# Performance work log

Hardware: AMD Instinct MI355X
Metric: run time of the kernel (lower is better)

Reference implementation:

```python
import jax, jax.numpy as jnp
import numpy as np

N0_SRC, N0_DST, E0 = 495616, 45056, 450560
N1_DST, E1 = 4096, 40960
IN_FEATS, N_HIDDEN, N_CLASSES = 256, 128, 16


def setup_inputs() -> dict:
    key = jax.random.key(0)
    ks = jax.random.split(key, 12)
    x = jax.random.normal(ks[0], (N0_SRC, IN_FEATS), dtype=jnp.float32)
    src0 = jax.random.randint(ks[1], (E0,), 0, N0_SRC, dtype=jnp.int32)
    dst0 = jax.random.randint(ks[2], (E0,), 0, N0_DST, dtype=jnp.int32)
    w0 = jax.random.uniform(ks[3], (E0,), dtype=jnp.float32)
    src1 = jax.random.randint(ks[4], (E1,), 0, N0_DST, dtype=jnp.int32)
    dst1 = jax.random.randint(ks[5], (E1,), 0, N1_DST, dtype=jnp.int32)
    w1 = jax.random.uniform(ks[6], (E1,), dtype=jnp.float32)
    # xavier-uniform-ish init for linear weights
    def xavier(k, shape):
        fan_out, fan_in = shape
        lim = jnp.sqrt(6.0 / (fan_in + fan_out))
        return jax.random.uniform(k, shape, jnp.float32, -lim, lim)
    return {
        "x": x, "src0": src0, "dst0": dst0, "w0": w0,
        "src1": src1, "dst1": dst1, "w1": w1,
        "Wn0": xavier(ks[7], (N_HIDDEN, IN_FEATS)), "bn0": jnp.zeros((N_HIDDEN,), jnp.float32),
        "Wn1": xavier(ks[8], (N_HIDDEN, N_HIDDEN)), "bn1": jnp.zeros((N_HIDDEN,), jnp.float32),
        "Wfc": xavier(ks[9], (N_CLASSES, N_HIDDEN)), "bfc": jnp.zeros((N_CLASSES,), jnp.float32),
        "ndst0": N0_DST, "ndst1": N1_DST,
    }


def _weighted_sage_gcn(h, src, dst, w, Wn, bn, num_dst):
    """DGL-style 'gcn' SAGEConv with edge weights on a bipartite block.

    dst nodes are the prefix h[:num_dst] of the src node set.
    h_out = relu(fc_neigh((sum_e w_e*h[src_e] + h_dst) / (sum_e w_e + 1)))
    """
    h_dst = h[:num_dst]
    msg = h[src] * w[:, None]                                   # [E, D]
    agg = jax.ops.segment_sum(msg, dst, num_segments=num_dst)   # [num_dst, D]
    deg = jax.ops.segment_sum(w, dst, num_segments=num_dst)     # [num_dst]
    h_neigh = (agg + h_dst) / (deg[:, None] + 1.0)
    return jax.nn.relu(h_neigh @ Wn.T + bn)


def reference(x, src0, dst0, w0, src1, dst1, w1, Wn0, bn0, Wn1, bn1, Wfc, bfc, ndst0, ndst1):
    h = _weighted_sage_gcn(x, src0, dst0, w0, Wn0, bn0, ndst0)
    h = _weighted_sage_gcn(h, src1, dst1, w1, Wn1, bn1, ndst1)
    return h @ Wfc.T + bfc  # [ndst1, n_classes]
```

## Files before the change

kernel.cpp:

```cpp
#include <hip/hip_runtime.h>

#define N0_SRC 495616
#define N0_DST 45056
#define E0 450560
#define N1_DST 4096
#define E1 40960
#define IN_FEATS 256
#define NH 128
#define NC 16

__global__ void hist_kernel(const int* __restrict__ dst, int* __restrict__ cnt) {
    int e = blockIdx.x * blockDim.x + threadIdx.x;
    if (e < E0) atomicAdd(&cnt[dst[e]], 1);
}

__global__ void __launch_bounds__(1024) scan_kernel(int* __restrict__ cnt,
                                                    int* __restrict__ row_start) {
    __shared__ int partial[1024];
    const int CH = N0_DST / 1024;
    int t = threadIdx.x;
    int base = t * CH;
    int s = 0;
    for (int j = 0; j < CH; j++) s += cnt[base + j];
    partial[t] = s;
    __syncthreads();
    for (int off = 1; off < 1024; off <<= 1) {
        int v = (t >= off) ? partial[t - off] : 0;
        __syncthreads();
        partial[t] += v;
        __syncthreads();
    }
    int run = partial[t] - s;
    for (int j = 0; j < CH; j++) {
        int c = cnt[base + j];
        row_start[base + j] = run;
        cnt[base + j] = run;
        run += c;
    }
    if (t == 1023) row_start[N0_DST] = run;
}

__global__ void scatter_kernel(const int* __restrict__ dst, const int* __restrict__ src,
                               const float* __restrict__ w, int* __restrict__ cursor,
                               int2* __restrict__ sw) {
    int e = blockIdx.x * blockDim.x + threadIdx.x;
    if (e < E0) {
        int p = atomicAdd(&cursor[dst[e]], 1);
        sw[p] = make_int2(src[e], __float_as_int(w[e]));
    }
}

__global__ void __launch_bounds__(256) agg0_kernel(const float* __restrict__ x,
    const int2* __restrict__ sw, const int* __restrict__ row_start,
    float* __restrict__ hneigh) {
    int wv = blockIdx.x * 4 + (threadIdx.x >> 6);
    int lane = threadIdx.x & 63;
    if (wv >= N0_DST) return;
    int beg = row_start[wv], end = row_start[wv + 1];
    const float4* x4 = (const float4*)x;
    float4 xd = x4[(size_t)wv * 64 + lane];
    float ax = 0.f, ay = 0.f, az = 0.f, aw = 0.f, degs = 0.f;
    for (int i = beg; i < end; i += 4) {
        int last = end - 1;
        int i1 = (i + 1 < end) ? i + 1 : last;
        int i2 = (i + 2 < end) ? i + 2 : last;
        int i3 = (i + 3 < end) ? i + 3 : last;
        int2 p0 = sw[i];
        int2 p1 = sw[i1];
        int2 p2 = sw[i2];
        int2 p3 = sw[i3];
        float4 v0 = x4[(size_t)p0.x * 64 + lane];
        float4 v1 = x4[(size_t)p1.x * 64 + lane];
        float4 v2 = x4[(size_t)p2.x * 64 + lane];
        float4 v3 = x4[(size_t)p3.x * 64 + lane];
        float w0 = __int_as_float(p0.y);
        float w1 = (i + 1 < end) ? __int_as_float(p1.y) : 0.f;
        float w2 = (i + 2 < end) ? __int_as_float(p2.y) : 0.f;
        float w3 = (i + 3 < end) ? __int_as_float(p3.y) : 0.f;
        ax = fmaf(w0, v0.x, ax); ay = fmaf(w0, v0.y, ay);
        az = fmaf(w0, v0.z, az); aw = fmaf(w0, v0.w, aw);
        ax = fmaf(w1, v1.x, ax); ay = fmaf(w1, v1.y, ay);
        az = fmaf(w1, v1.z, az); aw = fmaf(w1, v1.w, aw);
        ax = fmaf(w2, v2.x, ax); ay = fmaf(w2, v2.y, ay);
        az = fmaf(w2, v2.z, az); aw = fmaf(w2, v2.w, aw);
        ax = fmaf(w3, v3.x, ax); ay = fmaf(w3, v3.y, ay);
        az = fmaf(w3, v3.z, az); aw = fmaf(w3, v3.w, aw);
        degs += w0 + w1 + w2 + w3;
    }
    float inv = 1.0f / (degs + 1.0f);
    float4 r;
    r.x = (ax + xd.x) * inv; r.y = (ay + xd.y) * inv;
    r.z = (az + xd.z) * inv; r.w = (aw + xd.w) * inv;
    ((float4*)hneigh)[(size_t)wv * 64 + lane] = r;
}

__global__ void __launch_bounds__(128) gemm0_kernel(const float* __restrict__ hneigh,
    const float* __restrict__ Wn, const float* __restrict__ bn,
    float* __restrict__ h0) {
    __shared__ float hn[16][IN_FEATS];
    int nb = blockIdx.x * 16;
    int tid = threadIdx.x;
    const float4* s4 = (const float4*)(hneigh + (size_t)nb * IN_FEATS);
    float4* l4 = (float4*)&hn[0][0];
    for (int i = tid; i < 16 * IN_FEATS / 4; i += 128) l4[i] = s4[i];
    __syncthreads();
    float acc[16];
#pragma unroll
    for (int n = 0; n < 16; n++) acc[n] = 0.f;
    const float4* wr4 = (const float4*)(Wn + (size_t)tid * IN_FEATS);
#pragma unroll 4
    for (int k4 = 0; k4 < IN_FEATS / 4; k4++) {
        float4 wv = wr4[k4];
        int k = k4 * 4;
#pragma unroll
        for (int n = 0; n < 16; n++) {
            acc[n] += hn[n][k + 0] * wv.x;
            acc[n] += hn[n][k + 1] * wv.y;
            acc[n] += hn[n][k + 2] * wv.z;
            acc[n] += hn[n][k + 3] * wv.w;
        }
    }
    float b = bn[tid];
#pragma unroll
    for (int n = 0; n < 16; n++) {
        float v = acc[n] + b;
        h0[(size_t)(nb + n) * NH + tid] = v > 0.f ? v : 0.f;
    }
}

__global__ void edge1_kernel(const float* __restrict__ h0,
                             const int* __restrict__ src, const int* __restrict__ dst,
                             const float* __restrict__ w,
                             float* __restrict__ agg, float* __restrict__ deg) {
    int t = blockIdx.x * blockDim.x + threadIdx.x;
    int e = t >> 5;
    int lane = t & 31;
    if (e >= E1) return;
    int s = src[e], d = dst[e];
    float we = w[e];
    float4 v = ((const float4*)(h0 + (size_t)s * NH))[lane];
    float* ad = agg + (size_t)d * NH + lane * 4;
    unsafeAtomicAdd(ad + 0, v.x * we);
    unsafeAtomicAdd(ad + 1, v.y * we);
    unsafeAtomicAdd(ad + 2, v.z * we);
    unsafeAtomicAdd(ad + 3, v.w * we);
    if (lane == 0) unsafeAtomicAdd(deg + d, we);
}

__global__ void __launch_bounds__(128) gemm1_kernel(const float* __restrict__ h0,
    const float* __restrict__ agg, const float* __restrict__ deg,
    const float* __restrict__ Wn, const float* __restrict__ bn,
    float* __restrict__ h1) {
    __shared__ float hn[8][NH];
    int nb = blockIdx.x * 8;
    int tid = threadIdx.x;
    for (int i = tid; i < 8 * NH; i += 128) {
        int n = i >> 7;
        int k = i & 127;
        int m = nb + n;
        float hv = agg[(size_t)m * NH + k] + h0[(size_t)m * NH + k];
        hn[n][k] = hv / (deg[m] + 1.0f);
    }
    __syncthreads();
    float acc[8];
#pragma unroll
    for (int n = 0; n < 8; n++) acc[n] = 0.f;
    const float4* wr4 = (const float4*)(Wn + (size_t)tid * NH);
#pragma unroll 4
    for (int k4 = 0; k4 < NH / 4; k4++) {
        float4 wv = wr4[k4];
        int k = k4 * 4;
#pragma unroll
        for (int n = 0; n < 8; n++) {
            acc[n] += hn[n][k + 0] * wv.x;
            acc[n] += hn[n][k + 1] * wv.y;
            acc[n] += hn[n][k + 2] * wv.z;
            acc[n] += hn[n][k + 3] * wv.w;
        }
    }
    float b = bn[tid];
#pragma unroll
    for (int n = 0; n < 8; n++) {
        float v = acc[n] + b;
        h1[(size_t)(nb + n) * NH + tid] = v > 0.f ? v : 0.f;
    }
}

__global__ void fc_kernel(const float* __restrict__ h1, const float* __restrict__ Wfc,
                          const float* __restrict__ bfc, float* __restrict__ out) {
    int t = blockIdx.x * blockDim.x + threadIdx.x;
    int m = t >> 4, c = t & 15;
    if (m >= N1_DST) return;
    const float* hr = h1 + (size_t)m * NH;
    const float* wr = Wfc + (size_t)c * NH;
    float acc = 0.f;
    for (int k = 0; k < NH; k++) acc += hr[k] * wr[k];
    out[t] = acc + bfc[c];
}

extern "C" void kernel_launch(void* const* d_in, const int* in_sizes, int n_in,
                              void* d_out, int out_size, void* d_ws, size_t ws_size,
                              hipStream_t stream) {
    const float* x   = (const float*)d_in[0];
    const int* src0  = (const int*)d_in[1];
    const int* dst0  = (const int*)d_in[2];
    const float* w0  = (const float*)d_in[3];
    const int* src1  = (const int*)d_in[4];
    const int* dst1  = (const int*)d_in[5];
    const float* w1  = (const float*)d_in[6];
    const float* Wn0 = (const float*)d_in[7];
    const float* bn0 = (const float*)d_in[8];
    const float* Wn1 = (const float*)d_in[9];
    const float* bn1 = (const float*)d_in[10];
    const float* Wfc = (const float*)d_in[11];
    const float* bfc = (const float*)d_in[12];
    float* out = (float*)d_out;

    float* ws = (float*)d_ws;
    float* agg1      = ws;
    float* deg1      = agg1 + (size_t)N1_DST * NH;
    int*   cnt       = (int*)(deg1 + N1_DST);
    int*   row_start = cnt + N0_DST;
    float* hneigh    = ws + 618500;
    float* h0        = ws + 12152836;
    int2*  sw        = (int2*)h0;
    float* h1        = hneigh;

    size_t zero_floats = (size_t)N1_DST * NH + N1_DST + N0_DST;
    hipMemsetAsync(d_ws, 0, zero_floats * sizeof(float), stream);

    hist_kernel<<<(E0 + 255) / 256, 256, 0, stream>>>(dst0, cnt);
    scan_kernel<<<1, 1024, 0, stream>>>(cnt, row_start);
    scatter_kernel<<<(E0 + 255) / 256, 256, 0, stream>>>(dst0, src0, w0, cnt, sw);

    agg0_kernel<<<(N0_DST + 3) / 4, 256, 0, stream>>>(x, sw, row_start, hneigh);
    gemm0_kernel<<<N0_DST / 16, 128, 0, stream>>>(hneigh, Wn0, bn0, h0);

    edge1_kernel<<<(E1 * 32) / 256, 256, 0, stream>>>(h0, src1, dst1, w1, agg1, deg1);
    gemm1_kernel<<<N1_DST / 8, 128, 0, stream>>>(h0, agg1, deg1, Wn1, bn1, h1);

    fc_kernel<<<(N1_DST * NC) / 256, 256, 0, stream>>>(h1, Wfc, bfc, out);
}
```

Baseline: 905.9 us.

## Vectorize CSR build kernels, add tail loop in agg0, double gemm0 row tile

The histogram, scan and scatter kernels now load their inputs as int4/float4 and do four edges per thread. The agg0 gather loop gets a clean unrolled main body plus a scalar tail, so padding loads are no longer issued. gemm0 processes 32 rows per block instead of 16 to reuse each weight load across more rows, and fc uses float4 loads. The larger accumulator array raises register pressure in gemm0, and fewer threads issue the atomics.

```diff
diff --git a/kernel.cpp b/kernel.cpp
--- a/kernel.cpp
+++ b/kernel.cpp
@@ -9,9 +9,15 @@
 #define NH 128
 #define NC 16
 
-__global__ void hist_kernel(const int* __restrict__ dst, int* __restrict__ cnt) {
-    int e = blockIdx.x * blockDim.x + threadIdx.x;
-    if (e < E0) atomicAdd(&cnt[dst[e]], 1);
+__global__ void hist_kernel(const int4* __restrict__ dst4, int* __restrict__ cnt) {
+    int t = blockIdx.x * blockDim.x + threadIdx.x;
+    if (t < E0 / 4) {
+        int4 d = dst4[t];
+        atomicAdd(&cnt[d.x], 1);
+        atomicAdd(&cnt[d.y], 1);
+        atomicAdd(&cnt[d.z], 1);
+        atomicAdd(&cnt[d.w], 1);
+    }
 }
 
 __global__ void __launch_bounds__(1024) scan_kernel(int* __restrict__ cnt,
@@ -20,8 +26,13 @@
     const int CH = N0_DST / 1024;
     int t = threadIdx.x;
     int base = t * CH;
+    const int4* c4 = (const int4*)(cnt + base);
     int s = 0;
-    for (int j = 0; j < CH; j++) s += cnt[base + j];
+#pragma unroll
+    for (int j = 0; j < CH / 4; j++) {
+        int4 c = c4[j];
+        s += c.x + c.y + c.z + c.w;
+    }
     partial[t] = s;
     __syncthreads();
     for (int off = 1; off < 1024; off <<= 1) {
@@ -31,22 +42,38 @@
         __syncthreads();
     }
     int run = partial[t] - s;
-    for (int j = 0; j < CH; j++) {
-        int c = cnt[base + j];
-        row_start[base + j] = run;
-        cnt[base + j] = run;
-        run += c;
+    int4* r4 = (int4*)(row_start + base);
+    int4* u4 = (int4*)(cnt + base);
+#pragma unroll
+    for (int j = 0; j < CH / 4; j++) {
+        int4 c = c4[j];
+        int4 r;
+        r.x = run; run += c.x;
+        r.y = run; run += c.y;
+        r.z = run; run += c.z;
+        r.w = run; run += c.w;
+        r4[j] = r;
+        u4[j] = r;
     }
     if (t == 1023) row_start[N0_DST] = run;
 }
 
-__global__ void scatter_kernel(const int* __restrict__ dst, const int* __restrict__ src,
-                               const float* __restrict__ w, int* __restrict__ cursor,
+__global__ void scatter_kernel(const int4* __restrict__ dst4, const int4* __restrict__ src4,
+                               const float4* __restrict__ w4, int* __restrict__ cursor,
                                int2* __restrict__ sw) {
-    int e = blockIdx.x * blockDim.x + threadIdx.x;
-    if (e < E0) {
-        int p = atomicAdd(&cursor[dst[e]], 1);
-        sw[p] = make_int2(src[e], __float_as_int(w[e]));
+    int t = blockIdx.x * blockDim.x + threadIdx.x;
+    if (t < E0 / 4) {
+        int4 d = dst4[t];
+        int4 sc = src4[t];
+        float4 w = w4[t];
+        int p0 = atomicAdd(&cursor[d.x], 1);
+        sw[p0] = make_int2(sc.x, __float_as_int(w.x));
+        int p1 = atomicAdd(&cursor[d.y], 1);
+        sw[p1] = make_int2(sc.y, __float_as_int(w.y));
+        int p2 = atomicAdd(&cursor[d.z], 1);
+        sw[p2] = make_int2(sc.z, __float_as_int(w.z));
+        int p3 = atomicAdd(&cursor[d.w], 1);
+        sw[p3] = make_int2(sc.w, __float_as_int(w.w));
     }
 }
 
@@ -60,23 +87,20 @@
     const float4* x4 = (const float4*)x;
     float4 xd = x4[(size_t)wv * 64 + lane];
     float ax = 0.f, ay = 0.f, az = 0.f, aw = 0.f, degs = 0.f;
-    for (int i = beg; i < end; i += 4) {
-        int last = end - 1;
-        int i1 = (i + 1 < end) ? i + 1 : last;
-        int i2 = (i + 2 < end) ? i + 2 : last;
-        int i3 = (i + 3 < end) ? i + 3 : last;
+    int i = beg;
+    for (; i + 4 <= end; i += 4) {
         int2 p0 = sw[i];
-        int2 p1 = sw[i1];
-        int2 p2 = sw[i2];
-        int2 p3 = sw[i3];
+        int2 p1 = sw[i + 1];
+        int2 p2 = sw[i + 2];
+        int2 p3 = sw[i + 3];
         float4 v0 = x4[(size_t)p0.x * 64 + lane];
         float4 v1 = x4[(size_t)p1.x * 64 + lane];
         float4 v2 = x4[(size_t)p2.x * 64 + lane];
         float4 v3 = x4[(size_t)p3.x * 64 + lane];
         float w0 = __int_as_float(p0.y);
-        float w1 = (i + 1 < end) ? __int_as_float(p1.y) : 0.f;
-        float w2 = (i + 2 < end) ? __int_as_float(p2.y) : 0.f;
-        float w3 = (i + 3 < end) ? __int_as_float(p3.y) : 0.f;
+        float w1 = __int_as_float(p1.y);
+        float w2 = __int_as_float(p2.y);
+        float w3 = __int_as_float(p3.y);
         ax = fmaf(w0, v0.x, ax); ay = fmaf(w0, v0.y, ay);
         az = fmaf(w0, v0.z, az); aw = fmaf(w0, v0.w, aw);
         ax = fmaf(w1, v1.x, ax); ay = fmaf(w1, v1.y, ay);
@@ -87,6 +111,14 @@
         az = fmaf(w3, v3.z, az); aw = fmaf(w3, v3.w, aw);
         degs += w0 + w1 + w2 + w3;
     }
+    for (; i < end; i++) {
+        int2 p = sw[i];
+        float4 v = x4[(size_t)p.x * 64 + lane];
+        float w = __int_as_float(p.y);
+        ax = fmaf(w, v.x, ax); ay = fmaf(w, v.y, ay);
+        az = fmaf(w, v.z, az); aw = fmaf(w, v.w, aw);
+        degs += w;
+    }
     float inv = 1.0f / (degs + 1.0f);
     float4 r;
     r.x = (ax + xd.x) * inv; r.y = (ay + xd.y) * inv;
@@ -97,23 +129,23 @@
 __global__ void __launch_bounds__(128) gemm0_kernel(const float* __restrict__ hneigh,
     const float* __restrict__ Wn, const float* __restrict__ bn,
     float* __restrict__ h0) {
-    __shared__ float hn[16][IN_FEATS];
-    int nb = blockIdx.x * 16;
+    __shared__ float hn[32][IN_FEATS];
+    int nb = blockIdx.x * 32;
     int tid = threadIdx.x;
     const float4* s4 = (const float4*)(hneigh + (size_t)nb * IN_FEATS);
     float4* l4 = (float4*)&hn[0][0];
-    for (int i = tid; i < 16 * IN_FEATS / 4; i += 128) l4[i] = s4[i];
+    for (int i = tid; i < 32 * IN_FEATS / 4; i += 128) l4[i] = s4[i];
     __syncthreads();
-    float acc[16];
-#pragma unroll
-    for (int n = 0; n < 16; n++) acc[n] = 0.f;
+    float acc[32];
+#pragma unroll
+    for (int n = 0; n < 32; n++) acc[n] = 0.f;
     const float4* wr4 = (const float4*)(Wn + (size_t)tid * IN_FEATS);
-#pragma unroll 4
+#pragma unroll 2
     for (int k4 = 0; k4 < IN_FEATS / 4; k4++) {
         float4 wv = wr4[k4];
         int k = k4 * 4;
 #pragma unroll
-        for (int n = 0; n < 16; n++) {
+        for (int n = 0; n < 32; n++) {
             acc[n] += hn[n][k + 0] * wv.x;
             acc[n] += hn[n][k + 1] * wv.y;
             acc[n] += hn[n][k + 2] * wv.z;
@@ -122,7 +154,7 @@
     }
     float b = bn[tid];
 #pragma unroll
-    for (int n = 0; n < 16; n++) {
+    for (int n = 0; n < 32; n++) {
         float v = acc[n] + b;
         h0[(size_t)(nb + n) * NH + tid] = v > 0.f ? v : 0.f;
     }
@@ -191,10 +223,15 @@
     int t = blockIdx.x * blockDim.x + threadIdx.x;
     int m = t >> 4, c = t & 15;
     if (m >= N1_DST) return;
-    const float* hr = h1 + (size_t)m * NH;
-    const float* wr = Wfc + (size_t)c * NH;
+    const float4* hr = (const float4*)(h1 + (size_t)m * NH);
+    const float4* wr = (const float4*)(Wfc + (size_t)c * NH);
     float acc = 0.f;
-    for (int k = 0; k < NH; k++) acc += hr[k] * wr[k];
+#pragma unroll 8
+    for (int k = 0; k < NH / 4; k++) {
+        float4 a = hr[k];
+        float4 b = wr[k];
+        acc += a.x * b.x + a.y * b.y + a.z * b.z + a.w * b.w;
+    }
     out[t] = acc + bfc[c];
 }
 
@@ -229,12 +266,13 @@
     size_t zero_floats = (size_t)N1_DST * NH + N1_DST + N0_DST;
     hipMemsetAsync(d_ws, 0, zero_floats * sizeof(float), stream);
 
-    hist_kernel<<<(E0 + 255) / 256, 256, 0, stream>>>(dst0, cnt);
+    hist_kernel<<<(E0 / 4 + 255) / 256, 256, 0, stream>>>((const int4*)dst0, cnt);
     scan_kernel<<<1, 1024, 0, stream>>>(cnt, row_start);
-    scatter_kernel<<<(E0 + 255) / 256, 256, 0, stream>>>(dst0, src0, w0, cnt, sw);
+    scatter_kernel<<<(E0 / 4 + 255) / 256, 256, 0, stream>>>(
+        (const int4*)dst0, (const int4*)src0, (const float4*)w0, cnt, sw);
 
     agg0_kernel<<<(N0_DST + 3) / 4, 256, 0, stream>>>(x, sw, row_start, hneigh);
-    gemm0_kernel<<<N0_DST / 16, 128, 0, stream>>>(hneigh, Wn0, bn0, h0);
+    gemm0_kernel<<<N0_DST / 32, 128, 0, stream>>>(hneigh, Wn0, bn0, h0);
 
     edge1_kernel<<<(E1 * 32) / 256, 256, 0, stream>>>(h0, src1, dst1, w1, agg1, deg1);
     gemm1_kernel<<<N1_DST / 8, 128, 0, stream>>>(h0, agg1, deg1, Wn1, bn1, h1);
```

Result: slower. 946.4 us (+4.5%).
